# Kernel optimization log

Hardware: AMD Instinct MI355X
Metric: run time of the kernel (lower is better)

The kernel has to match this reference:

```python
import jax, jax.numpy as jnp
import numpy as np
from math import sqrt

N = 8192      # points
I = 16        # in_channels
H = 64        # hidden_units
O = 64        # out_channels
CUTS = 8      # conv MLP intermediate width
RADIUS = 9.0
GROUPS = 4    # GroupNorm groups
BLK = 128     # i-block size for tiled pairwise reduction (KeOps-style)


def _leaky(x):
    return jnp.where(x >= 0, x, 0.2 * x)


def _group_norm(f, w, b, eps=1e-5):
    # torch GroupNorm applied to (1, C, N): stats per group over (C//G channels x N points)
    n, c = f.shape
    g = f.reshape(n, GROUPS, c // GROUPS)
    m = g.mean(axis=(0, 2), keepdims=True)
    v = ((g - m) ** 2).mean(axis=(0, 2), keepdims=True)
    g = (g - m) * jax.lax.rsqrt(v + eps)
    return g.reshape(n, c) * w + b


def setup_inputs() -> dict:
    key = jax.random.key(0)
    ks = jax.random.split(key, 20)
    U = lambda k, s, lim: jax.random.uniform(k, s, minval=-lim, maxval=lim)
    points = jax.random.normal(ks[0], (N, 3), dtype=jnp.float32)
    nuv = jax.random.normal(ks[1], (N, 3, 3), dtype=jnp.float32)
    features = jax.random.normal(ks[2], (N, I), dtype=jnp.float32)
    # net_in (torch Linear default init)
    W_in1 = U(ks[3], (H, I), 1 / np.sqrt(I)); b_in1 = U(ks[4], (H,), 1 / np.sqrt(I))
    W_in2 = U(ks[5], (H, H), 1 / np.sqrt(H)); b_in2 = U(ks[6], (H,), 1 / np.sqrt(H))
    # conv MLP with custom init from the module
    A1 = jax.random.normal(ks[7], (CUTS, 3), dtype=jnp.float32)
    B1 = jax.random.uniform(ks[8], (CUTS,)) * 0.8 * jnp.sqrt((A1 ** 2).sum(-1))
    A2 = U(ks[9], (H, CUTS), 1 / np.sqrt(CUTS))
    B2 = jax.random.normal(ks[10], (H,)) * 0.5 * jnp.sqrt((A2 ** 2).sum(-1))
    # net_out
    W_out1 = U(ks[11], (O, H), 1 / np.sqrt(H)); b_out1 = U(ks[12], (O,), 1 / np.sqrt(H))
    W_out2 = U(ks[13], (O, O), 1 / np.sqrt(O)); b_out2 = U(ks[14], (O,), 1 / np.sqrt(O))
    return {
        "points": points, "nuv": nuv, "features": features,
        "W_in1": W_in1, "b_in1": b_in1, "W_in2": W_in2, "b_in2": b_in2,
        "gn_in_w": jnp.ones((H,), jnp.float32), "gn_in_b": jnp.zeros((H,), jnp.float32),
        "A1": A1, "B1": B1, "A2": A2, "B2": B2,
        "W_out1": W_out1, "b_out1": b_out1, "W_out2": W_out2, "b_out2": b_out2,
        "gn_out_w": jnp.ones((O,), jnp.float32), "gn_out_b": jnp.zeros((O,), jnp.float32),
    }


def _forward(points, nuv, features, W_in1, b_in1, W_in2, b_in2, gn_in_w, gn_in_b,
             A1, B1, A2, B2, W_out1, b_out1, W_out2, b_out2, gn_out_w, gn_out_b):
    # 1. net_in + GroupNorm
    f = _leaky(features @ W_in1.T + b_in1)
    f = _leaky(f @ W_in2.T + b_in2)
    f = _group_norm(f, gn_in_w, gn_in_b)          # (N, H)
    # 2. quasi-geodesic interaction, tiled over i-blocks (KeOps-style)
    pts = points / (sqrt(2.0) * RADIUS)
    normals = jax.lax.stop_gradient(nuv[:, 0, :])  # n_j is detached in the original
    nblk = N // BLK

    def body(carry, blk):
        xi, nuvi = blk                              # (B,3), (B,3,3)
        ni = nuvi[:, 0, :]                          # (B,3) n_i (not detached)
        diff = pts[None, :, :] - xi[:, None, :]     # (B,N,3) x_j - x_i
        dn = ni @ normals.T                         # (B,N) <n_i, n_j>
        d2 = (diff ** 2).sum(-1) * (2.0 - dn) ** 2  # pseudo-geodesic squared dist
        w = jnp.exp(-d2)                            # Gaussian window
        X = jnp.einsum('bij,bnj->bni', nuvi, diff)  # coords in local basis (B,N,3)
        h = jax.nn.relu(jnp.einsum('bnj,cj->bnc', X, A1) + B1)   # (B,N,CUTS)
        g = jax.nn.relu(jnp.einsum('bnc,hc->bnh', h, A2) + B2)   # (B,N,H)
        out = jnp.einsum('bn,bnh,nh->bh', w, g, f)  # sum_j w_ij * conv(P_ij) * f_j
        return carry, out

    _, outs = jax.lax.scan(
        body, None, (pts.reshape(nblk, BLK, 3), nuv.reshape(nblk, BLK, 3, 3)))
    f2 = outs.reshape(N, H)
    # 3. net_out + GroupNorm
    f2 = _leaky(f2 @ W_out1.T + b_out1)
    f2 = _leaky(f2 @ W_out2.T + b_out2)
    f2 = _group_norm(f2, gn_out_w, gn_out_b)       # (N, O)
    return f2


def reference(points, nuv, features, W_in1, b_in1, W_in2, b_in2, gn_in_w, gn_in_b,
              A1, B1, A2, B2, W_out1, b_out1, W_out2, b_out2, gn_out_w, gn_out_b):
    return _forward(points, nuv, features, W_in1, b_in1, W_in2, b_in2, gn_in_w, gn_in_b,
                    A1, B1, A2, B2, W_out1, b_out1, W_out2, b_out2, gn_out_w, gn_out_b)
```

## Files before the change

### kernel.cpp

```cpp
#include <hip/hip_runtime.h>
#include <hip/hip_bf16.h>
#include <stdint.h>


#define N_PTS   8192
#define CHUNK   64
#define NCHUNK  (N_PTS / CHUNK)
#define WPB     8
#define PSCALE  0.07856742013183861f
#define GN_CNT  (N_PTS * 16)
#define FS_STRIDE 68

#define OFF_POINTS 0
#define OFF_NUV    24576
#define OFF_FEAT   98304
#define OFF_WIN1   229376
#define OFF_BIN1   230400
#define OFF_WIN2   230464
#define OFF_BIN2   234560
#define OFF_GNIW   234624
#define OFF_GNIB   234688
#define OFF_A1     234752
#define OFF_B1     234776
#define OFF_A2     234784
#define OFF_B2     235296
#define OFF_WOUT1  235360
#define OFF_BOUT1  239456
#define OFF_WOUT2  239520
#define OFF_BOUT2  243616
#define OFF_GNOW   243680
#define OFF_GNOB   243744
#define CVT_TOTAL  243808
#define NSEG 19

typedef _Float16 half2_t __attribute__((ext_vector_type(2)));
typedef _Float16 f16x4   __attribute__((ext_vector_type(4)));
typedef float    f32x2   __attribute__((ext_vector_type(2)));
typedef float    f32x4   __attribute__((ext_vector_type(4)));

struct InPtrs { const void* p[NSEG]; };

__device__ __forceinline__ float rfl(float x) {
  return __int_as_float(__builtin_amdgcn_readfirstlane(__float_as_int(x)));
}
__device__ __forceinline__ float leaky(float x) { return x > 0.f ? x : 0.2f * x; }

#if __has_builtin(__builtin_amdgcn_cvt_pkrtz)
__device__ __forceinline__ half2_t pk16(float a, float b) {
  return __builtin_bit_cast(half2_t, __builtin_amdgcn_cvt_pkrtz(a, b));
}
#else
__device__ __forceinline__ half2_t pk16(float a, float b) {
  half2_t r; r.x = (_Float16)a; r.y = (_Float16)b; return r;
}
#endif

__global__ __launch_bounds__(256) void prep_kernel(InPtrs ptrs, float* dst,
                                                   float* gstats) {
  if (blockIdx.x == 0 && threadIdx.x < 16) gstats[threadIdx.x] = 0.f;
  const uint32_t w0 = ((const uint32_t*)ptrs.p[7])[0];
  const bool bf = (w0 != 0x3F800000u);
  const int CUM[NSEG + 1] = {0, 24576, 98304, 229376, 230400, 230464, 234560,
                             234624, 234688, 234752, 234776, 234784, 235296,
                             235360, 239456, 239520, 243616, 243680, 243744,
                             243808};
  for (int e = blockIdx.x * 256 + threadIdx.x; e < CVT_TOTAL;
       e += gridDim.x * 256) {
    int s = 0;
#pragma unroll
    for (int i = 1; i < NSEG; ++i) s += (e >= CUM[i]) ? 1 : 0;
    const int rem = e - CUM[s];
    float v = bf ? __bfloat162float(((const __hip_bfloat16*)ptrs.p[s])[rem])
                 : ((const float*)ptrs.p[s])[rem];
    if (s == 0) v *= PSCALE;
    dst[e] = v;
  }
}

__global__ __launch_bounds__(256) void pack_kernel(
    const float* __restrict__ pool, float4* __restrict__ ppk,
    float4* __restrict__ npk) {
  const int n = blockIdx.x * 256 + threadIdx.x;
  const float px = pool[OFF_POINTS + n * 3 + 0];
  const float py = pool[OFF_POINTS + n * 3 + 1];
  const float pz = pool[OFF_POINTS + n * 3 + 2];
  float4 p; p.x = px; p.y = py; p.z = pz;
  p.w = fmaf(px, px, fmaf(py, py, pz * pz));
  ppk[n] = p;
  float4 q;
  q.x = pool[OFF_NUV + n * 9 + 0];
  q.y = pool[OFF_NUV + n * 9 + 1];
  q.z = pool[OFF_NUV + n * 9 + 2];
  q.w = 0.f;
  npk[n] = q;
}

__global__ __launch_bounds__(256) void mlp_in_kernel(
    const float* __restrict__ pool, float* __restrict__ fbuf) {
  __shared__ float ls[4][64];
  const int t = threadIdx.x, nl = t >> 6, h = t & 63;
  const int n = blockIdx.x * 4 + nl;
  const float4* fr = (const float4*)(pool + OFF_FEAT + n * 16);
  const float4* w1 = (const float4*)(pool + OFF_WIN1 + h * 16);
  float a = pool[OFF_BIN1 + h];
#pragma unroll
  for (int k = 0; k < 4; ++k) {
    const float4 x = fr[k], w = w1[k];
    a = fmaf(x.x, w.x, a); a = fmaf(x.y, w.y, a);
    a = fmaf(x.z, w.z, a); a = fmaf(x.w, w.w, a);
  }
  ls[nl][h] = leaky(a);
  __syncthreads();
  const float4* w2 = (const float4*)(pool + OFF_WIN2 + h * 64);
  const float4* lr = (const float4*)&ls[nl][0];
  float c = pool[OFF_BIN2 + h];
#pragma unroll
  for (int k = 0; k < 16; ++k) {
    const float4 x = lr[k], w = w2[k];
    c = fmaf(x.x, w.x, c); c = fmaf(x.y, w.y, c);
    c = fmaf(x.z, w.z, c); c = fmaf(x.w, w.w, c);
  }
  fbuf[n * 64 + h] = leaky(c);
}

__global__ __launch_bounds__(256) void mlp_out_kernel(
    const float* __restrict__ cbuf, const float* __restrict__ pool,
    float* __restrict__ obuf) {
  __shared__ float ls[4][64];
  const int t = threadIdx.x, nl = t >> 6, h = t & 63;
  const int n = blockIdx.x * 4 + nl;
  const float4* cr = (const float4*)(cbuf + n * 64);
  const float4* w1 = (const float4*)(pool + OFF_WOUT1 + h * 64);
  float a = pool[OFF_BOUT1 + h];
#pragma unroll
  for (int k = 0; k < 16; ++k) {
    const float4 x = cr[k], w = w1[k];
    a = fmaf(x.x, w.x, a); a = fmaf(x.y, w.y, a);
    a = fmaf(x.z, w.z, a); a = fmaf(x.w, w.w, a);
  }
  ls[nl][h] = leaky(a);
  __syncthreads();
  const float4* w2 = (const float4*)(pool + OFF_WOUT2 + h * 64);
  const float4* lr = (const float4*)&ls[nl][0];
  float c = pool[OFF_BOUT2 + h];
#pragma unroll
  for (int k = 0; k < 16; ++k) {
    const float4 x = lr[k], w = w2[k];
    c = fmaf(x.x, w.x, c); c = fmaf(x.y, w.y, c);
    c = fmaf(x.z, w.z, c); c = fmaf(x.w, w.w, c);
  }
  obuf[n * 64 + h] = leaky(c);
}

__global__ __launch_bounds__(256) void gn_stats_kernel(
    const float* __restrict__ buf, float* __restrict__ gstats) {
  __shared__ float red[8];
  const int t = threadIdx.x;
  const int g = (t & 63) >> 4;
  if (t < 8) red[t] = 0.f;
  float s = 0.f, q = 0.f;
  for (int idx = blockIdx.x * 256 + t; idx < N_PTS * 64; idx += 64 * 256) {
    const float v = buf[idx];
    s += v; q = fmaf(v, v, q);
  }
  __syncthreads();
  atomicAdd(&red[g], s);
  atomicAdd(&red[4 + g], q);
  __syncthreads();
  if (t < 8) atomicAdd(&gstats[t], red[t]);
}

__global__ __launch_bounds__(256) void gn_apply_kernel(
    float* __restrict__ buf, const float* __restrict__ gstats,
    const float* __restrict__ pool) {
  const int idx = blockIdx.x * 256 + threadIdx.x;
  const int h = idx & 63, g = h >> 4;
  const float m = gstats[g] * (1.f / GN_CNT);
  const float v = gstats[4 + g] * (1.f / GN_CNT) - m * m;
  const float rs = rsqrtf(fmaxf(v, 0.f) + 1e-5f);
  buf[idx] = fmaf((buf[idx] - m) * rs, pool[OFF_GNIW + h], pool[OFF_GNIB + h]);
}

__global__ __launch_bounds__(256) void gn_apply_out_kernel(
    const float* __restrict__ buf, const float* __restrict__ gstats,
    const float* __restrict__ pool, void* __restrict__ out,
    const uint32_t* __restrict__ dref) {
  const bool bf = (dref[0] != 0x3F800000u);
  const int idx = blockIdx.x * 256 + threadIdx.x;
  const int h = idx & 63, g = h >> 4;
  const float m = gstats[g] * (1.f / GN_CNT);
  const float v = gstats[4 + g] * (1.f / GN_CNT) - m * m;
  const float rs = rsqrtf(fmaxf(v, 0.f) + 1e-5f);
  const float r = fmaf((buf[idx] - m) * rs, pool[OFF_GNOW + h], pool[OFF_GNOB + h]);
  if (bf) ((__hip_bfloat16*)out)[idx] = __float2bfloat16(r);
  else    ((float*)out)[idx] = r;
}

__global__ __launch_bounds__(512, 4) void conv_kernel(
    const float* __restrict__ pool, const float* __restrict__ fbuf,
    float* __restrict__ cbuf, const float4* __restrict__ ppk,
    const float4* __restrict__ npk) {
  __shared__ float  f_s[CHUNK * FS_STRIDE];
  __shared__ float4 hcA2[WPB][CHUNK];
  __shared__ f32x2  hcW2[WPB][CHUNK];
  __shared__ f32x2  zero2_s;

  const int t = threadIdx.x;
  const int wv = t >> 6, lane = t & 63;
  const int b = blockIdx.x * WPB + wv;
  const int kg  = lane >> 4;
  const int l15 = lane & 15;

  const float pbx = rfl(pool[OFF_POINTS + b * 3 + 0]);
  const float pby = rfl(pool[OFF_POINTS + b * 3 + 1]);
  const float pbz = rfl(pool[OFF_POINTS + b * 3 + 2]);
  float nb[9];
#pragma unroll
  for (int i = 0; i < 9; ++i) nb[i] = rfl(pool[OFF_NUV + b * 9 + i]);
  const float pbsq = rfl(fmaf(pbx, pbx, fmaf(pby, pby, pbz * pbz)));

  float mM[24], mc[8];
#pragma unroll
  for (int cc = 0; cc < 8; ++cc) {
    const float a0 = pool[OFF_A1 + cc * 3 + 0];
    const float a1 = pool[OFF_A1 + cc * 3 + 1];
    const float a2 = pool[OFF_A1 + cc * 3 + 2];
#pragma unroll
    for (int j = 0; j < 3; ++j)
      mM[cc * 3 + j] =
          rfl(fmaf(a0, nb[j], fmaf(a1, nb[3 + j], a2 * nb[6 + j])));
    mc[cc] = rfl(fmaf(-mM[cc * 3 + 0], pbx,
                 fmaf(-mM[cc * 3 + 1], pby,
                 fmaf(-mM[cc * 3 + 2], pbz, pool[OFF_B1 + cc]))));
  }

  f16x4 bfrag[4];
#pragma unroll
  for (int ht = 0; ht < 4; ++ht) {
    const int h = 16 * ht + l15;
#pragma unroll
    for (int i = 0; i < 4; ++i) {
      const int k = 4 * kg + i;
      float v = 0.f;
      if (k < 8) v = pool[OFF_A2 + h * 8 + k];
      else if (k == 8) v = pool[OFF_B2 + h];
      bfrag[ht][i] = (_Float16)v;
    }
  }

  if (t == 0) { zero2_s.x = 0.f; zero2_s.y = 0.f; }

  f32x2 acc01[4], acc23[4];
#pragma unroll
  for (int ht = 0; ht < 4; ++ht) {
    acc01[ht].x = 0.f; acc01[ht].y = 0.f;
    acc23[ht].x = 0.f; acc23[ht].y = 0.f;
  }
  const f32x4 kzero = {0.f, 0.f, 0.f, 0.f};
  const float4* fg4 = (const float4*)fbuf;

  float4 fv0 = fg4[t];
  float4 fv1 = fg4[t + 512];
  float4 pv  = ppk[lane];
  float4 nv  = npk[lane];

  for (int c = 0; c < NCHUNK; ++c) {
    asm volatile("" ::: "memory");
    __builtin_amdgcn_s_barrier();
    asm volatile("" ::: "memory");

    ((float4*)f_s)[(t >> 4) * 17 + (t & 15)]        = fv0;
    ((float4*)f_s)[((t >> 4) + 32) * 17 + (t & 15)] = fv1;

    const float dotp = fmaf(pv.x, pbx, fmaf(pv.y, pby, pv.z * pbz));
    const float dd   = fmaf(-2.f, dotp, pv.w + pbsq);
    const float dn   = fmaf(nb[0], nv.x, fmaf(nb[1], nv.y, nb[2] * nv.z));
    const float ttv  = 2.f - dn;
    const float wexp = __expf(-dd * ttv * ttv);
    float hc[8];
#pragma unroll
    for (int cc = 0; cc < 8; ++cc)
      hc[cc] = wexp * fmaxf(fmaf(mM[cc * 3 + 0], pv.x,
                            fmaf(mM[cc * 3 + 1], pv.y,
                            fmaf(mM[cc * 3 + 2], pv.z, mc[cc]))), 0.f);
    float4 av;
    av.x = __builtin_bit_cast(float, pk16(hc[0], hc[1]));
    av.y = __builtin_bit_cast(float, pk16(hc[2], hc[3]));
    av.z = __builtin_bit_cast(float, pk16(hc[4], hc[5]));
    av.w = __builtin_bit_cast(float, pk16(hc[6], hc[7]));
    hcA2[wv][lane] = av;
    f32x2 wv2;
    wv2.x = __builtin_bit_cast(float, pk16(wexp, 0.f));
    wv2.y = 0.f;
    hcW2[wv][lane] = wv2;

    const int cn = (c < NCHUNK - 1) ? c + 1 : c;
    fv0 = fg4[cn * 1024 + t];
    fv1 = fg4[cn * 1024 + t + 512];
    pv  = ppk[cn * CHUNK + lane];
    nv  = npk[cn * CHUNK + lane];

    asm volatile("s_waitcnt lgkmcnt(0)" ::: "memory");
    __builtin_amdgcn_s_barrier();
    asm volatile("" ::: "memory");

#pragma unroll
    for (int jt = 0; jt < 4; ++jt) {
      const f32x2* ap;
      if (kg < 2)       ap = ((const f32x2*)&hcA2[wv][16 * jt + l15]) + kg;
      else if (kg == 2) ap = &hcW2[wv][16 * jt + l15];
      else              ap = &zero2_s;
      const f16x4 af = __builtin_bit_cast(f16x4, *ap);
      const int fbase = (16 * jt + kg * 4) * FS_STRIDE + l15;
#pragma unroll
      for (int ht = 0; ht < 4; ++ht) {
        const f32x4 D = __builtin_amdgcn_mfma_f32_16x16x16f16(
            af, bfrag[ht], kzero, 0, 0, 0);
        const float* fb = &f_s[fbase + 16 * ht];
        f32x2 fq01, fq23, q01, q23;
        fq01.x = fb[0];             fq01.y = fb[FS_STRIDE];
        fq23.x = fb[2 * FS_STRIDE]; fq23.y = fb[3 * FS_STRIDE];
        q01.x = fmaxf(D[0], 0.f);   q01.y = fmaxf(D[1], 0.f);
        q23.x = fmaxf(D[2], 0.f);   q23.y = fmaxf(D[3], 0.f);
        asm("v_pk_fma_f32 %0, %1, %2, %0"
            : "+v"(acc01[ht]) : "v"(fq01), "v"(q01));
        asm("v_pk_fma_f32 %0, %1, %2, %0"
            : "+v"(acc23[ht]) : "v"(fq23), "v"(q23));
      }
    }
  }

  float accf[4];
#pragma unroll
  for (int ht = 0; ht < 4; ++ht) {
    float a = (acc01[ht].x + acc01[ht].y) + (acc23[ht].x + acc23[ht].y);
    a += __shfl_xor(a, 16, 64);
    a += __shfl_xor(a, 32, 64);
    accf[ht] = a;
  }
  if (lane < 16) {
#pragma unroll
    for (int ht = 0; ht < 4; ++ht)
      cbuf[b * 64 + 16 * ht + lane] = accf[ht];
  }
}

extern "C" void kernel_launch(void* const* d_in, const int* in_sizes, int n_in,
                              void* d_out, int out_size, void* d_ws, size_t ws_size,
                              hipStream_t stream) {
  (void)in_sizes; (void)n_in; (void)out_size; (void)ws_size;
  const uint32_t* dref = (const uint32_t*)d_in[7];

  float* pool   = (float*)d_ws;
  float* fbuf   = pool + CVT_TOTAL;
  float* cbuf   = fbuf + N_PTS * 64;
  float* gstats = cbuf + N_PTS * 64;
  float* ppk    = gstats + 16;
  float* npk    = ppk + N_PTS * 4;

  InPtrs ptrs;
  for (int i = 0; i < NSEG; ++i) ptrs.p[i] = d_in[i];

  prep_kernel<<<256, 256, 0, stream>>>(ptrs, pool, gstats);
  pack_kernel<<<N_PTS / 256, 256, 0, stream>>>(pool, (float4*)ppk, (float4*)npk);
  mlp_in_kernel<<<N_PTS / 4, 256, 0, stream>>>(pool, fbuf);
  gn_stats_kernel<<<64, 256, 0, stream>>>(fbuf, gstats);
  gn_apply_kernel<<<N_PTS * 64 / 256, 256, 0, stream>>>(fbuf, gstats, pool);
  conv_kernel<<<N_PTS / WPB, 512, 0, stream>>>(pool, fbuf, cbuf,
                                               (const float4*)ppk,
                                               (const float4*)npk);
  mlp_out_kernel<<<N_PTS / 4, 256, 0, stream>>>(cbuf, pool, fbuf);
  gn_stats_kernel<<<64, 256, 0, stream>>>(fbuf, gstats + 8);
  gn_apply_out_kernel<<<N_PTS * 64 / 256, 256, 0, stream>>>(
      fbuf, gstats + 8, pool, d_out, dref);
}
```

Before: 754.2 us.

## Pre-swizzle normalized features into MFMA fragment order and use K=32 MFMA

The GroupNorm apply kernel now writes the normalized features already permuted into per-chunk MFMA output-fragment order. The conv kernel can then fill shared memory with plain float4 copies and read one float4 per fragment instead of four strided scalars. The conv MFMA moves from 16x16x16 to 16x16x32 f16, packing the hidden taps plus the bias row into one K=32 operand, and the software prefetch of the next chunk is replaced by loads at the top of each iteration. The explicit occupancy hint is also dropped. Risks are reduced latency hiding without prefetch, extra padded zero lanes in the MFMA, and different register pressure and occupancy.

```diff
diff --git a/kernel.cpp b/kernel.cpp
--- a/kernel.cpp
+++ b/kernel.cpp
@@ -9,7 +9,6 @@
 #define WPB     8
 #define PSCALE  0.07856742013183861f
 #define GN_CNT  (N_PTS * 16)
-#define FS_STRIDE 68
 
 #define OFF_POINTS 0
 #define OFF_NUV    24576
@@ -34,7 +33,7 @@
 #define NSEG 19
 
 typedef _Float16 half2_t __attribute__((ext_vector_type(2)));
-typedef _Float16 f16x4   __attribute__((ext_vector_type(4)));
+typedef _Float16 f16x8   __attribute__((ext_vector_type(8)));
 typedef float    f32x2   __attribute__((ext_vector_type(2)));
 typedef float    f32x4   __attribute__((ext_vector_type(4)));
 
@@ -170,15 +169,47 @@
   if (t < 8) atomicAdd(&gstats[t], red[t]);
 }
 
-__global__ __launch_bounds__(256) void gn_apply_kernel(
-    float* __restrict__ buf, const float* __restrict__ gstats,
-    const float* __restrict__ pool) {
-  const int idx = blockIdx.x * 256 + threadIdx.x;
-  const int h = idx & 63, g = h >> 4;
+__global__ __launch_bounds__(256) void gn_apply_Q_kernel(
+    const float* __restrict__ buf, const float* __restrict__ gstats,
+    const float* __restrict__ pool, float4* __restrict__ bufq) {
+  __shared__ float tile[64][68];
+  const int t = threadIdx.x;
+  const int c = blockIdx.x;
+  const int n0 = c * 64;
+  const int rr = t >> 4;
+  const int cc4 = (t & 15) * 4;
+  const int g = cc4 >> 4;
   const float m = gstats[g] * (1.f / GN_CNT);
   const float v = gstats[4 + g] * (1.f / GN_CNT) - m * m;
   const float rs = rsqrtf(fmaxf(v, 0.f) + 1e-5f);
-  buf[idx] = fmaf((buf[idx] - m) * rs, pool[OFF_GNIW + h], pool[OFF_GNIB + h]);
+  const float4 gw = *(const float4*)&pool[OFF_GNIW + cc4];
+  const float4 gb = *(const float4*)&pool[OFF_GNIB + cc4];
+#pragma unroll
+  for (int r = 0; r < 4; ++r) {
+    const int row = rr + 16 * r;
+    const float4 x = *(const float4*)&buf[(n0 + row) * 64 + cc4];
+    float4 o;
+    o.x = fmaf((x.x - m) * rs, gw.x, gb.x);
+    o.y = fmaf((x.y - m) * rs, gw.y, gb.y);
+    o.z = fmaf((x.z - m) * rs, gw.z, gb.z);
+    o.w = fmaf((x.w - m) * rs, gw.w, gb.w);
+    *(float4*)&tile[row][cc4] = o;
+  }
+  __syncthreads();
+#pragma unroll
+  for (int si = 0; si < 4; ++si) {
+    const int s = t + 256 * si;
+    const int region = s >> 6, lane = s & 63;
+    const int jt = region >> 2, ht = region & 3;
+    const int kg = lane >> 4, l15 = lane & 15;
+    const int jb = 16 * jt + 4 * kg, h = 16 * ht + l15;
+    float4 o;
+    o.x = tile[jb + 0][h];
+    o.y = tile[jb + 1][h];
+    o.z = tile[jb + 2][h];
+    o.w = tile[jb + 3][h];
+    bufq[c * 1024 + s] = o;
+  }
 }
 
 __global__ __launch_bounds__(256) void gn_apply_out_kernel(
@@ -196,14 +227,13 @@
   else    ((float*)out)[idx] = r;
 }
 
-__global__ __launch_bounds__(512, 4) void conv_kernel(
-    const float* __restrict__ pool, const float* __restrict__ fbuf,
+__global__ __launch_bounds__(512) void conv_kernel(
+    const float* __restrict__ pool, const float4* __restrict__ fq,
     float* __restrict__ cbuf, const float4* __restrict__ ppk,
     const float4* __restrict__ npk) {
-  __shared__ float  f_s[CHUNK * FS_STRIDE];
-  __shared__ float4 hcA2[WPB][CHUNK];
-  __shared__ f32x2  hcW2[WPB][CHUNK];
-  __shared__ f32x2  zero2_s;
+  __shared__ float4 f_q[1024];
+  __shared__ float4 hcA[WPB][4][32];
+  __shared__ float4 zero4_s;
 
   const int t = threadIdx.x;
   const int wv = t >> 6, lane = t & 63;
@@ -234,43 +264,45 @@
                  fmaf(-mM[cc * 3 + 2], pbz, pool[OFF_B1 + cc]))));
   }
 
-  f16x4 bfrag[4];
+  f16x8 bfrag[4];
 #pragma unroll
   for (int ht = 0; ht < 4; ++ht) {
     const int h = 16 * ht + l15;
 #pragma unroll
-    for (int i = 0; i < 4; ++i) {
-      const int k = 4 * kg + i;
+    for (int i = 0; i < 8; ++i) {
       float v = 0.f;
-      if (k < 8) v = pool[OFF_A2 + h * 8 + k];
-      else if (k == 8) v = pool[OFF_B2 + h];
+      if (kg == 0) v = pool[OFF_A2 + h * 8 + i];
+      else if (kg == 1 && i == 0) v = pool[OFF_B2 + h];
       bfrag[ht][i] = (_Float16)v;
     }
   }
 
-  if (t == 0) { zero2_s.x = 0.f; zero2_s.y = 0.f; }
-
+  {
+    float4 z4; z4.x = 0.f; z4.y = 0.f; z4.z = 0.f; z4.w = 0.f;
+    if (lane < 32) {
+#pragma unroll
+      for (int jt = 0; jt < 4; ++jt) hcA[wv][jt][lane] = z4;
+    }
+    if (t == 0) zero4_s = z4;
+  }
+
+  const f32x4 kzero = {0.f, 0.f, 0.f, 0.f};
   f32x2 acc01[4], acc23[4];
 #pragma unroll
   for (int ht = 0; ht < 4; ++ht) {
     acc01[ht].x = 0.f; acc01[ht].y = 0.f;
     acc23[ht].x = 0.f; acc23[ht].y = 0.f;
   }
-  const f32x4 kzero = {0.f, 0.f, 0.f, 0.f};
-  const float4* fg4 = (const float4*)fbuf;
-
-  float4 fv0 = fg4[t];
-  float4 fv1 = fg4[t + 512];
-  float4 pv  = ppk[lane];
-  float4 nv  = npk[lane];
 
   for (int c = 0; c < NCHUNK; ++c) {
-    asm volatile("" ::: "memory");
-    __builtin_amdgcn_s_barrier();
-    asm volatile("" ::: "memory");
-
-    ((float4*)f_s)[(t >> 4) * 17 + (t & 15)]        = fv0;
-    ((float4*)f_s)[((t >> 4) + 32) * 17 + (t & 15)] = fv1;
+    const float4 fv0 = fq[c * 1024 + t];
+    const float4 fv1 = fq[c * 1024 + t + 512];
+    const float4 pv = ppk[c * CHUNK + lane];
+    const float4 nv = npk[c * CHUNK + lane];
+
+    __syncthreads();
+    f_q[t]       = fv0;
+    f_q[t + 512] = fv1;
 
     const float dotp = fmaf(pv.x, pbx, fmaf(pv.y, pby, pv.z * pbz));
     const float dd   = fmaf(-2.f, dotp, pv.w + pbsq);
@@ -283,45 +315,31 @@
       hc[cc] = wexp * fmaxf(fmaf(mM[cc * 3 + 0], pv.x,
                             fmaf(mM[cc * 3 + 1], pv.y,
                             fmaf(mM[cc * 3 + 2], pv.z, mc[cc]))), 0.f);
-    float4 av;
-    av.x = __builtin_bit_cast(float, pk16(hc[0], hc[1]));
-    av.y = __builtin_bit_cast(float, pk16(hc[2], hc[3]));
-    av.z = __builtin_bit_cast(float, pk16(hc[4], hc[5]));
-    av.w = __builtin_bit_cast(float, pk16(hc[6], hc[7]));
-    hcA2[wv][lane] = av;
-    f32x2 wv2;
-    wv2.x = __builtin_bit_cast(float, pk16(wexp, 0.f));
-    wv2.y = 0.f;
-    hcW2[wv][lane] = wv2;
-
-    const int cn = (c < NCHUNK - 1) ? c + 1 : c;
-    fv0 = fg4[cn * 1024 + t];
-    fv1 = fg4[cn * 1024 + t + 512];
-    pv  = ppk[cn * CHUNK + lane];
-    nv  = npk[cn * CHUNK + lane];
-
-    asm volatile("s_waitcnt lgkmcnt(0)" ::: "memory");
-    __builtin_amdgcn_s_barrier();
-    asm volatile("" ::: "memory");
+    float4 lo;
+    lo.x = __builtin_bit_cast(float, pk16(hc[0], hc[1]));
+    lo.y = __builtin_bit_cast(float, pk16(hc[2], hc[3]));
+    lo.z = __builtin_bit_cast(float, pk16(hc[4], hc[5]));
+    lo.w = __builtin_bit_cast(float, pk16(hc[6], hc[7]));
+    hcA[wv][lane >> 4][l15] = lo;
+    ((float*)&hcA[wv][lane >> 4][16 + l15])[0] =
+        __builtin_bit_cast(float, pk16(wexp, 0.f));
+
+    __syncthreads();
 
 #pragma unroll
     for (int jt = 0; jt < 4; ++jt) {
-      const f32x2* ap;
-      if (kg < 2)       ap = ((const f32x2*)&hcA2[wv][16 * jt + l15]) + kg;
-      else if (kg == 2) ap = &hcW2[wv][16 * jt + l15];
-      else              ap = &zero2_s;
-      const f16x4 af = __builtin_bit_cast(f16x4, *ap);
-      const int fbase = (16 * jt + kg * 4) * FS_STRIDE + l15;
+      const float4* ap = (kg < 2) ? &hcA[wv][jt][kg * 16 + l15] : &zero4_s;
+      const f16x8 af = __builtin_bit_cast(f16x8, *ap);
 #pragma unroll
       for (int ht = 0; ht < 4; ++ht) {
-        const f32x4 D = __builtin_amdgcn_mfma_f32_16x16x16f16(
+        const f32x4 D = __builtin_amdgcn_mfma_f32_16x16x32_f16(
             af, bfrag[ht], kzero, 0, 0, 0);
-        const float* fb = &f_s[fbase + 16 * ht];
+        const float4 fv = f_q[(jt * 4 + ht) * 64 + lane];
         f32x2 fq01, fq23, q01, q23;
-        fq01.x = fb[0];             fq01.y = fb[FS_STRIDE];
-        fq23.x = fb[2 * FS_STRIDE]; fq23.y = fb[3 * FS_STRIDE];
-        q01.x = fmaxf(D[0], 0.f);   q01.y = fmaxf(D[1], 0.f);
-        q23.x = fmaxf(D[2], 0.f);   q23.y = fmaxf(D[3], 0.f);
+        fq01.x = fv.x; fq01.y = fv.y;
+        fq23.x = fv.z; fq23.y = fv.w;
+        q01.x = fmaxf(D[0], 0.f); q01.y = fmaxf(D[1], 0.f);
+        q23.x = fmaxf(D[2], 0.f); q23.y = fmaxf(D[3], 0.f);
         asm("v_pk_fma_f32 %0, %1, %2, %0"
             : "+v"(acc01[ht]) : "v"(fq01), "v"(q01));
         asm("v_pk_fma_f32 %0, %1, %2, %0"
@@ -355,7 +373,8 @@
   float* fbuf   = pool + CVT_TOTAL;
   float* cbuf   = fbuf + N_PTS * 64;
   float* gstats = cbuf + N_PTS * 64;
-  float* ppk    = gstats + 16;
+  float* fbufq  = gstats + 16;
+  float* ppk    = fbufq + N_PTS * 64;
   float* npk    = ppk + N_PTS * 4;
 
   InPtrs ptrs;
@@ -365,9 +384,10 @@
   pack_kernel<<<N_PTS / 256, 256, 0, stream>>>(pool, (float4*)ppk, (float4*)npk);
   mlp_in_kernel<<<N_PTS / 4, 256, 0, stream>>>(pool, fbuf);
   gn_stats_kernel<<<64, 256, 0, stream>>>(fbuf, gstats);
-  gn_apply_kernel<<<N_PTS * 64 / 256, 256, 0, stream>>>(fbuf, gstats, pool);
-  conv_kernel<<<N_PTS / WPB, 512, 0, stream>>>(pool, fbuf, cbuf,
-                                               (const float4*)ppk,
+  gn_apply_Q_kernel<<<NCHUNK, 256, 0, stream>>>(fbuf, gstats, pool,
+                                                (float4*)fbufq);
+  conv_kernel<<<N_PTS / WPB, 512, 0, stream>>>(pool, (const float4*)fbufq,
+                                               cbuf, (const float4*)ppk,
                                                (const float4*)npk);
   mlp_out_kernel<<<N_PTS / 4, 256, 0, stream>>>(cbuf, pool, fbuf);
   gn_stats_kernel<<<64, 256, 0, stream>>>(fbuf, gstats + 8);
```

After: 697.9 us. 7.5% less time.
